# Kernel tuning notes

Measured on AMD Instinct MI355X. Metric: run time of the kernel, lower is better.

Reference implementation:

```python
import jax, jax.numpy as jnp
import numpy as np
from jax import lax

SCORE_THR = 0.1
IOU_THR = 0.3
NUM_CLASSES = 80
MAX_COORD = 4096.0  # class offset for class-aware NMS (boxes live in [0, ~1100])


def setup_inputs() -> dict:
    key = jax.random.key(0)
    bs, n = 4, 4096
    k1, k2, k3, k4 = jax.random.split(key, 4)
    # realistic boxes: centers in [0,1024], w/h in [10,210]
    cxcy = jax.random.uniform(k1, (bs, n, 2), minval=0.0, maxval=1024.0)
    wh = jax.random.uniform(k2, (bs, n, 2), minval=10.0, maxval=210.0)
    x1y1 = cxcy - wh * 0.5
    x2y2 = cxcy + wh * 0.5
    scores = jax.random.uniform(k3, (bs, n, 1), minval=0.0, maxval=1.0)
    cls = jax.random.randint(k4, (bs, n, 1), 0, NUM_CLASSES).astype(jnp.float32)
    batch_preds = jnp.concatenate([x1y1, x2y2, scores, cls], axis=-1)  # [bs, n, 6]
    return {"batch_preds": batch_preds}


def _iou_matrix(boxes):
    # boxes: [N, 4] (x1, y1, x2, y2) -> pairwise IoU [N, N]
    x1, y1, x2, y2 = boxes[:, 0], boxes[:, 1], boxes[:, 2], boxes[:, 3]
    area = (x2 - x1) * (y2 - y1)
    ix1 = jnp.maximum(x1[:, None], x1[None, :])
    iy1 = jnp.maximum(y1[:, None], y1[None, :])
    ix2 = jnp.minimum(x2[:, None], x2[None, :])
    iy2 = jnp.minimum(y2[:, None], y2[None, :])
    inter = jnp.maximum(ix2 - ix1, 0.0) * jnp.maximum(iy2 - iy1, 0.0)
    return inter / (area[:, None] + area[None, :] - inter + 1e-9)


def _nms_image(preds):
    # preds: [N, 6]. Returns preds zeroed where not kept (fixed-shape mask NMS).
    n = preds.shape[0]
    boxes, scores, cls = preds[:, :4], preds[:, 4], preds[:, 5]
    valid = scores >= SCORE_THR
    # class-aware trick == per-class NMS: offset boxes by class so cross-class IoU = 0
    obox = boxes + (cls * MAX_COORD)[:, None]
    order = jnp.argsort(-jnp.where(valid, scores, -jnp.inf))
    sboxes = obox[order]
    svalid = valid[order]
    iou = _iou_matrix(sboxes)  # [N, N]
    idxs = jnp.arange(n)

    def body(suppressed, inp):
        iou_row, v_i, i = inp
        keep_i = v_i & jnp.logical_not(suppressed[i])
        suppressed = suppressed | (keep_i & (iou_row > IOU_THR) & (idxs > i))
        return suppressed, keep_i

    _, keep_sorted = lax.scan(body, jnp.zeros((n,), bool), (iou, svalid, idxs))
    keep = jnp.zeros((n,), bool).at[order].set(keep_sorted)
    return preds * keep[:, None].astype(preds.dtype)


def reference(batch_preds):
    # Fixed-shape formulation of score filtering + per-class greedy NMS:
    # suppressed / below-threshold rows are zeroed instead of removed.
    return jax.vmap(_nms_image)(batch_preds)
```

## Files before the change

### kernel.cpp

```cpp
#include <hip/hip_runtime.h>
#include <hip/hip_bf16.h>

typedef unsigned long long u64;

#define BS 4
#define NBOX 4096
#define NCLS 80
#define CAPC 128
#define SCORE_THR 0.1f
#define IOU_THR 0.3f
#define MAX_COORD 4096.0f

__global__ __launch_bounds__(1024) void k_group(const float* __restrict__ preds,
                                                unsigned* __restrict__ clsIdx,
                                                unsigned* __restrict__ clsCnt,
                                                float* __restrict__ out) {
    __shared__ unsigned cur[NCLS];
    const int img = blockIdx.x;
    const int t = threadIdx.x;
    if (t < NCLS) cur[t] = 0;

    float4* oz = (float4*)(out + (size_t)img * NBOX * 6);
#pragma unroll
    for (int z = 0; z < 6; ++z)
        oz[t + z * 1024] = make_float4(0.f, 0.f, 0.f, 0.f);
    __syncthreads();

    const float* P = preds + (size_t)img * NBOX * 6;
#pragma unroll
    for (int r = 0; r < 4; ++r) {
        int e = t + r * 1024;
        float2 sc = *(const float2*)(P + (size_t)e * 6 + 4);
        if (sc.x >= SCORE_THR) {
            int c = (int)sc.y;
            unsigned slot = atomicAdd(&cur[c], 1u);
            if (slot < CAPC)
                clsIdx[((size_t)img * NCLS + c) * CAPC + slot] = (unsigned)e;
        }
    }
    __syncthreads();
    if (t < NCLS) clsCnt[img * NCLS + t] = min(cur[t], (unsigned)CAPC);
}

__global__ __launch_bounds__(64) void k_nms_cls(const float* __restrict__ preds,
                                               const unsigned* __restrict__ clsIdx,
                                               const unsigned* __restrict__ clsCnt,
                                               float* __restrict__ out) {
    __shared__ u64 skey[CAPC];
    __shared__ float4 sbx[CAPC];
    __shared__ unsigned sidx[CAPC];
    const int cls = blockIdx.x;
    const int img = blockIdx.y;
    const int lane = threadIdx.x;
    const int s = (int)clsCnt[img * NCLS + cls];
    if (s == 0) return;

    const float* P = preds + (size_t)img * NBOX * 6;
    float* O = out + (size_t)img * NBOX * 6;
    const unsigned* CI = clsIdx + ((size_t)img * NCLS + cls) * CAPC;

    u64 key[2];
    float4 bx[2] = {make_float4(0,0,0,0), make_float4(0,0,0,0)};
    unsigned oi[2] = {0, 0};
#pragma unroll
    for (int r = 0; r < 2; ++r) {
        int m = lane + 64 * r;
        key[r] = ~0ull;
        if (m < s) {
            unsigned e = CI[m];
            oi[r] = e;
            const float* R = P + (size_t)e * 6;
            float x1 = R[0], y1 = R[1], x2 = R[2], y2 = R[3], sc = R[4], cl = R[5];
            float off = cl * MAX_COORD;
            bx[r] = make_float4(x1 + off, y1 + off, x2 + off, y2 + off);
            unsigned u = __float_as_uint(sc);
            u = (u & 0x80000000u) ? ~u : (u | 0x80000000u);
            key[r] = ((u64)(~u) << 32) | (u64)e;
        }
        skey[m] = key[r];
    }
    __syncthreads();

    int rank[2] = {0, 0};
    for (int j = 0; j < s; ++j) {
        u64 kj = skey[j];
        rank[0] += (kj < key[0]);
        rank[1] += (kj < key[1]);
    }
    __syncthreads();
#pragma unroll
    for (int r = 0; r < 2; ++r) {
        int m = lane + 64 * r;
        if (m < s) { sbx[rank[r]] = bx[r]; sidx[rank[r]] = oi[r]; }
    }
    __syncthreads();

    float4 cb[2] = {make_float4(0,0,0,0), make_float4(0,0,0,0)};
    float ca[2] = {0.f, 0.f};
    unsigned coi[2] = {0, 0};
    bool removed[2];
#pragma unroll
    for (int r = 0; r < 2; ++r) {
        int c = lane + 64 * r;
        removed[r] = (c >= s);
        if (c < s) {
            cb[r] = sbx[c];
            coi[r] = sidx[c];
            ca[r] = (cb[r].z - cb[r].x) * (cb[r].w - cb[r].y);
        }
    }

    for (int i = 0; i < s; ++i) {
        u64 mA = __ballot(removed[0]);
        u64 mB = __ballot(removed[1]);
        u64 m = (i < 64) ? mA : mB;
        bool kept = !((m >> (i & 63)) & 1ull);
        if (kept) {
            float4 rb = sbx[i];
            float ra = (rb.z - rb.x) * (rb.w - rb.y);
#pragma unroll
            for (int r = 0; r < 2; ++r) {
                int c = lane + 64 * r;
                if (c > i && !removed[r]) {
                    float ix1 = fmaxf(rb.x, cb[r].x), iy1 = fmaxf(rb.y, cb[r].y);
                    float ix2 = fminf(rb.z, cb[r].z), iy2 = fminf(rb.w, cb[r].w);
                    float iw = fmaxf(ix2 - ix1, 0.f), ih = fmaxf(iy2 - iy1, 0.f);
                    float inter = iw * ih;
                    float iou = inter / (ra + ca[r] - inter + 1e-9f);
                    if (iou > IOU_THR) removed[r] = true;
                }
            }
        }
    }

#pragma unroll
    for (int r = 0; r < 2; ++r) {
        int c = lane + 64 * r;
        if (c < s && !removed[r]) {
            unsigned e = coi[r];
            const float* R = P + (size_t)e * 6;
            float* W = O + (size_t)e * 6;
#pragma unroll
            for (int q = 0; q < 6; ++q) W[q] = R[q];
        }
    }
}

extern "C" void kernel_launch(void* const* d_in, const int* in_sizes, int n_in,
                              void* d_out, int out_size, void* d_ws, size_t ws_size,
                              hipStream_t stream) {
    const float* preds = (const float*)d_in[0];
    float* out = (float*)d_out;

    unsigned* clsIdx = (unsigned*)d_ws;
    unsigned* clsCnt = clsIdx + (size_t)BS * NCLS * CAPC;

    k_group<<<BS, 1024, 0, stream>>>(preds, clsIdx, clsCnt, out);
    k_nms_cls<<<dim3(NCLS, BS), 64, 0, stream>>>(preds, clsIdx, clsCnt, out);
}
```

Baseline: 77.91 us.

## Fuse class grouping and per-class NMS into a single kernel

```diff
diff --git a/kernel.cpp b/kernel.cpp
--- a/kernel.cpp
+++ b/kernel.cpp
@@ -7,72 +7,68 @@
 #define NBOX 4096
 #define NCLS 80
 #define CAPC 128
+#define ZBLK 16
 #define SCORE_THR 0.1f
 #define IOU_THR 0.3f
 #define MAX_COORD 4096.0f
 
-__global__ __launch_bounds__(1024) void k_group(const float* __restrict__ preds,
-                                                unsigned* __restrict__ clsIdx,
-                                                unsigned* __restrict__ clsCnt,
+__global__ __launch_bounds__(64) void k_nms_all(const float* __restrict__ preds,
                                                 float* __restrict__ out) {
-    __shared__ unsigned cur[NCLS];
-    const int img = blockIdx.x;
-    const int t = threadIdx.x;
-    if (t < NCLS) cur[t] = 0;
+    const int img = blockIdx.y;
+    const int bx = blockIdx.x;
+    const int lane = threadIdx.x;
+    const float* P = preds + (size_t)img * NBOX * 6;
+    float* O = out + (size_t)img * NBOX * 6;
 
-    float4* oz = (float4*)(out + (size_t)img * NBOX * 6);
+    if (bx >= NCLS) {
+        const int base = (bx - NCLS) * (NBOX / ZBLK);
 #pragma unroll
-    for (int z = 0; z < 6; ++z)
-        oz[t + z * 1024] = make_float4(0.f, 0.f, 0.f, 0.f);
+        for (int r = 0; r < (NBOX / ZBLK) / 64; ++r) {
+            int e = base + lane + r * 64;
+            float sc = P[(size_t)e * 6 + 4];
+            if (sc < SCORE_THR) {
+                float* W = O + (size_t)e * 6;
+#pragma unroll
+                for (int q = 0; q < 6; ++q) W[q] = 0.0f;
+            }
+        }
+        return;
+    }
+
+    __shared__ unsigned mem[CAPC];
+    __shared__ unsigned scnt;
+    __shared__ u64 skey[CAPC];
+    __shared__ float4 sbx[CAPC];
+    __shared__ unsigned sidx[CAPC];
+    const int cls = bx;
+    if (lane == 0) scnt = 0;
     __syncthreads();
 
-    const float* P = preds + (size_t)img * NBOX * 6;
-#pragma unroll
-    for (int r = 0; r < 4; ++r) {
-        int e = t + r * 1024;
-        float2 sc = *(const float2*)(P + (size_t)e * 6 + 4);
-        if (sc.x >= SCORE_THR) {
-            int c = (int)sc.y;
-            unsigned slot = atomicAdd(&cur[c], 1u);
-            if (slot < CAPC)
-                clsIdx[((size_t)img * NCLS + c) * CAPC + slot] = (unsigned)e;
+    for (int m = lane; m < NBOX; m += 64) {
+        float2 sc = *(const float2*)(P + (size_t)m * 6 + 4);
+        if (sc.x >= SCORE_THR && (int)sc.y == cls) {
+            unsigned slot = atomicAdd(&scnt, 1u);
+            if (slot < CAPC) mem[slot] = (unsigned)m;
         }
     }
     __syncthreads();
-    if (t < NCLS) clsCnt[img * NCLS + t] = min(cur[t], (unsigned)CAPC);
-}
-
-__global__ __launch_bounds__(64) void k_nms_cls(const float* __restrict__ preds,
-                                               const unsigned* __restrict__ clsIdx,
-                                               const unsigned* __restrict__ clsCnt,
-                                               float* __restrict__ out) {
-    __shared__ u64 skey[CAPC];
-    __shared__ float4 sbx[CAPC];
-    __shared__ unsigned sidx[CAPC];
-    const int cls = blockIdx.x;
-    const int img = blockIdx.y;
-    const int lane = threadIdx.x;
-    const int s = (int)clsCnt[img * NCLS + cls];
+    const int s = (int)min(scnt, (unsigned)CAPC);
     if (s == 0) return;
 
-    const float* P = preds + (size_t)img * NBOX * 6;
-    float* O = out + (size_t)img * NBOX * 6;
-    const unsigned* CI = clsIdx + ((size_t)img * NCLS + cls) * CAPC;
-
     u64 key[2];
-    float4 bx[2] = {make_float4(0,0,0,0), make_float4(0,0,0,0)};
+    float4 bx2[2] = {make_float4(0,0,0,0), make_float4(0,0,0,0)};
     unsigned oi[2] = {0, 0};
 #pragma unroll
     for (int r = 0; r < 2; ++r) {
         int m = lane + 64 * r;
         key[r] = ~0ull;
         if (m < s) {
-            unsigned e = CI[m];
+            unsigned e = mem[m];
             oi[r] = e;
             const float* R = P + (size_t)e * 6;
             float x1 = R[0], y1 = R[1], x2 = R[2], y2 = R[3], sc = R[4], cl = R[5];
             float off = cl * MAX_COORD;
-            bx[r] = make_float4(x1 + off, y1 + off, x2 + off, y2 + off);
+            bx2[r] = make_float4(x1 + off, y1 + off, x2 + off, y2 + off);
             unsigned u = __float_as_uint(sc);
             u = (u & 0x80000000u) ? ~u : (u | 0x80000000u);
             key[r] = ((u64)(~u) << 32) | (u64)e;
@@ -91,7 +87,7 @@
 #pragma unroll
     for (int r = 0; r < 2; ++r) {
         int m = lane + 64 * r;
-        if (m < s) { sbx[rank[r]] = bx[r]; sidx[rank[r]] = oi[r]; }
+        if (m < s) { sbx[rank[r]] = bx2[r]; sidx[rank[r]] = oi[r]; }
     }
     __syncthreads();
 
@@ -136,12 +132,17 @@
 #pragma unroll
     for (int r = 0; r < 2; ++r) {
         int c = lane + 64 * r;
-        if (c < s && !removed[r]) {
+        if (c < s) {
             unsigned e = coi[r];
             const float* R = P + (size_t)e * 6;
             float* W = O + (size_t)e * 6;
+            if (!removed[r]) {
 #pragma unroll
-            for (int q = 0; q < 6; ++q) W[q] = R[q];
+                for (int q = 0; q < 6; ++q) W[q] = R[q];
+            } else {
+#pragma unroll
+                for (int q = 0; q < 6; ++q) W[q] = 0.0f;
+            }
         }
     }
 }
@@ -151,10 +152,5 @@
                               hipStream_t stream) {
     const float* preds = (const float*)d_in[0];
     float* out = (float*)d_out;
-
-    unsigned* clsIdx = (unsigned*)d_ws;
-    unsigned* clsCnt = clsIdx + (size_t)BS * NCLS * CAPC;
-
-    k_group<<<BS, 1024, 0, stream>>>(preds, clsIdx, clsCnt, out);
-    k_nms_cls<<<dim3(NCLS, BS), 64, 0, stream>>>(preds, clsIdx, clsCnt, out);
+    k_nms_all<<<dim3(NCLS + ZBLK, BS), 64, 0, stream>>>(preds, out);
 }
```

Result: slower. 90.89 us (+16.7%).
